# Optimization experiments

Hardware: AMD Instinct MI355X
Metric: run time of the kernel (lower is better)

Reference implementation:

```python
import jax, jax.numpy as jnp
import numpy as np

N = 65536
WAVE_SPEED = 1.0


def _mlp(pt, Ws, bs):
    # pt: [4] -> scalar. 6 tanh hidden layers of width 128, linear head.
    h = pt
    for W, b in zip(Ws[:-1], bs[:-1]):
        h = jnp.tanh(W @ h + b)
    return (Ws[-1] @ h + bs[-1])[0]


def setup_inputs() -> dict:
    key = jax.random.key(0)
    ks = jax.random.split(key, 32)
    d = {}
    for i, name in enumerate(["t", "x", "y", "z"]):
        d[name] = jax.random.normal(ks[i], (N,), dtype=jnp.float32)
    sizes = [(128, 4)] + [(128, 128)] * 5 + [(1, 128)]
    for i, (fan_out, fan_in) in enumerate(sizes):
        # Glorot-like scale for tanh MLP
        scale = np.float32(1.0 / np.sqrt(fan_in))
        d[f"W{i}"] = jax.random.normal(ks[4 + i], (fan_out, fan_in), dtype=jnp.float32) * scale
        d[f"b{i}"] = jnp.zeros((fan_out,), dtype=jnp.float32)
    return d


def reference(t, x, y, z, W0, b0, W1, b1, W2, b2, W3, b3, W4, b4, W5, b5, W6, b6):
    Ws = [W0, W1, W2, W3, W4, W5, W6]
    bs = [b0, b1, b2, b3, b4, b5, b6]

    def u(pt):
        return _mlp(pt, Ws, bs)

    def residual_point(pt):
        # Full 4x4 Hessian via forward-over-reverse; we need only the diagonal.
        H = jax.hessian(u)(pt)  # [4, 4]
        u_tt = H[0, 0]
        laplacian = H[1, 1] + H[2, 2] + H[3, 3]
        return u_tt - (WAVE_SPEED ** 2) * laplacian

    pts = jnp.stack([t, x, y, z], axis=-1)  # [N, 4]
    return jax.vmap(residual_point)(pts)  # [N]
```

## Files before the change

### kernel.cpp

```cpp
#include <hip/hip_runtime.h>
#include <hip/hip_fp16.h>
#include <math.h>


typedef _Float16 f16x8 __attribute__((ext_vector_type(8)));
typedef _Float16 f16x4 __attribute__((ext_vector_type(4)));
typedef _Float16 f16x2 __attribute__((ext_vector_type(2)));
typedef float    f32x4 __attribute__((ext_vector_type(4)));

constexpr int TPB  = 256;
constexpr int P    = 16;
constexpr int H    = 128;
constexpr int XPAD = 136;
constexpr int NV   = 6;
constexpr int WFRAG_HALVES = 5 * 8 * 4 * 64 * 8;
constexpr size_t WS_NEEDED = 2 * WFRAG_HALVES * sizeof(_Float16);

__device__ __forceinline__ float fast_tanh(float v) {
    float e = __expf(-2.0f * fabsf(v));
    float r = __builtin_amdgcn_rcpf(1.0f + e);
    return copysignf((1.0f - e) * r, v);
}

__device__ __forceinline__ f16x2 pkrtz(float a, float b) {
    return __builtin_bit_cast(f16x2, __builtin_amdgcn_cvt_pkrtz(a, b));
}

__global__ __launch_bounds__(256) void presplit_w(
    const float* __restrict__ W1, const float* __restrict__ W2,
    const float* __restrict__ W3, const float* __restrict__ W4,
    const float* __restrict__ W5, _Float16* __restrict__ whi,
    _Float16* __restrict__ wlo)
{
    const int gid = blockIdx.x * 256 + threadIdx.x;
    const float* Ws[5] = { W1, W2, W3, W4, W5 };
    const int lane = gid & 63;
    const int rest = gid >> 6;
    const int ks   = rest & 3;
    const int mt   = (rest >> 2) & 7;
    const int l    = rest >> 5;
    const int n    = mt * 16 + (lane & 15);
    const int k0   = ks * 32 + (lane >> 4) * 8;
    const float4 u0 = *(const float4*)&Ws[l][n * H + k0];
    const float4 u1 = *(const float4*)&Ws[l][n * H + k0 + 4];
    const float vv[8] = { u0.x, u0.y, u0.z, u0.w, u1.x, u1.y, u1.z, u1.w };
    f16x8 h, o;
    #pragma unroll
    for (int e = 0; e < 8; ++e) {
        _Float16 hh = (_Float16)vv[e];
        h[e] = hh;
        o[e] = (_Float16)(vv[e] - (float)hh);
    }
    *(f16x8*)&whi[gid * 8] = h;
    *(f16x8*)&wlo[gid * 8] = o;
}

__global__ __launch_bounds__(TPB, 3) void pinn_mfma5(
    const float* __restrict__ t, const float* __restrict__ x,
    const float* __restrict__ y, const float* __restrict__ z,
    const float* __restrict__ W0, const float* __restrict__ b0,
    const float* __restrict__ W1, const float* __restrict__ b1,
    const float* __restrict__ W2, const float* __restrict__ b2,
    const float* __restrict__ W3, const float* __restrict__ b3,
    const float* __restrict__ W4, const float* __restrict__ b4,
    const float* __restrict__ W5, const float* __restrict__ b5,
    const float* __restrict__ W6,
    const _Float16* __restrict__ whi, const _Float16* __restrict__ wlo,
    int use_pre, float* __restrict__ out, int N)
{
    __shared__ _Float16 sXhi[NV * P * XPAD];
    __shared__ _Float16 sXlo[NV * P * XPAD];
    __shared__ float    sRed[4][P];

    const int tid  = threadIdx.x;
    const int lane = tid & 63;
    const int wn   = tid >> 6;
    const int l15  = lane & 15;
    const int l4   = lane >> 4;
    const int gb   = blockIdx.x * P;

    {
        const int p0 = tid >> 4;
        const int i0 = tid & 15;
        int gp = gb + p0; if (gp >= N) gp = N - 1;
        const float pt0 = t[gp], pt1 = x[gp], pt2 = y[gp], pt3 = z[gp];
        float nv[NV][8];
        #pragma unroll
        for (int j = 0; j < 8; ++j) {
            const int i = i0 * 8 + j;
            const float4 wv = *(const float4*)&W0[i * 4];
            const float zv = fmaf(wv.x, pt0, fmaf(wv.y, pt1, fmaf(wv.z, pt2, fmaf(wv.w, pt3, b0[i]))));
            const float hv = fast_tanh(zv);
            const float s  = 1.0f - hv * hv;
            const float ssq = ((wv.x * wv.x - wv.y * wv.y) - wv.z * wv.z) - wv.w * wv.w;
            nv[0][j] = hv;       nv[1][j] = s * wv.x; nv[2][j] = s * wv.y;
            nv[3][j] = s * wv.z; nv[4][j] = s * wv.w; nv[5][j] = -2.0f * hv * s * ssq;
        }
        #pragma unroll
        for (int v = 0; v < NV; ++v) {
            f16x8 hh, oo;
            #pragma unroll
            for (int j = 0; j < 8; ++j) {
                _Float16 h_ = (_Float16)nv[v][j];
                hh[j] = h_;
                oo[j] = (_Float16)(nv[v][j] - (float)h_);
            }
            const int off = (v * P + p0) * XPAD + i0 * 8;
            *(f16x8*)&sXhi[off] = hh;
            *(f16x8*)&sXlo[off] = oo;
        }
    }
    __syncthreads();

    const float* Wl[5] = { W1, W2, W3, W4, W5 };
    const float* bl[5] = { b1, b2, b3, b4, b5 };

    for (int l = 0; l < 5; ++l) {
        f32x4 acc[NV][2];
        #pragma unroll
        for (int v = 0; v < NV; ++v)
            #pragma unroll
            for (int nt = 0; nt < 2; ++nt) acc[v][nt] = (f32x4){0.f, 0.f, 0.f, 0.f};

        const float* __restrict__ Wc = Wl[l];

        #pragma unroll
        for (int ks = 0; ks < 4; ++ks) {
            f16x8 ah[2], al[2];
            if (use_pre) {
                #pragma unroll
                for (int nt = 0; nt < 2; ++nt) {
                    const int f = ((l * 8 + (wn * 2 + nt)) * 4 + ks) * 64 + lane;
                    ah[nt] = *(const f16x8*)&whi[f * 8];
                    al[nt] = *(const f16x8*)&wlo[f * 8];
                }
            } else {
                #pragma unroll
                for (int nt = 0; nt < 2; ++nt) {
                    const int n  = (wn * 2 + nt) * 16 + l15;
                    const int k0 = ks * 32 + l4 * 8;
                    const float4 u0 = *(const float4*)&Wc[n * H + k0];
                    const float4 u1 = *(const float4*)&Wc[n * H + k0 + 4];
                    const float vv[8] = { u0.x, u0.y, u0.z, u0.w, u1.x, u1.y, u1.z, u1.w };
                    #pragma unroll
                    for (int e = 0; e < 8; ++e) {
                        _Float16 h_ = (_Float16)vv[e];
                        ah[nt][e] = h_;
                        al[nt][e] = (_Float16)(vv[e] - (float)h_);
                    }
                }
            }
            f16x8 xh[NV], xl[NV];
            #pragma unroll
            for (int v = 0; v < NV; ++v) {
                const int base = (v * P + l15) * XPAD + ks * 32 + l4 * 8;
                xh[v] = *(const f16x8*)&sXhi[base];
                xl[v] = *(const f16x8*)&sXlo[base];
            }
            __builtin_amdgcn_s_setprio(1);
            #pragma unroll
            for (int v = 0; v < NV; ++v)
                #pragma unroll
                for (int nt = 0; nt < 2; ++nt)
                    acc[v][nt] = __builtin_amdgcn_mfma_f32_16x16x32_f16(ah[nt], xh[v], acc[v][nt], 0, 0, 0);
            #pragma unroll
            for (int v = 0; v < NV; ++v)
                #pragma unroll
                for (int nt = 0; nt < 2; ++nt)
                    acc[v][nt] = __builtin_amdgcn_mfma_f32_16x16x32_f16(ah[nt], xl[v], acc[v][nt], 0, 0, 0);
            #pragma unroll
            for (int v = 0; v < NV; ++v)
                #pragma unroll
                for (int nt = 0; nt < 2; ++nt)
                    acc[v][nt] = __builtin_amdgcn_mfma_f32_16x16x32_f16(al[nt], xh[v], acc[v][nt], 0, 0, 0);
            __builtin_amdgcn_s_setprio(0);
        }
        __syncthreads();

        if (l < 4) {
            const float* __restrict__ bc = bl[l];
            #pragma unroll
            for (int nt = 0; nt < 2; ++nt) {
                const int n0 = (wn * 2 + nt) * 16 + l4 * 4;
                const float4 b4v = *(const float4*)&bc[n0];
                const float bb[4] = { b4v.x, b4v.y, b4v.z, b4v.w };
                float nv[NV][4];
                #pragma unroll
                for (int r = 0; r < 4; ++r) {
                    const float zv = acc[0][nt][r] + bb[r];
                    const float hv = fast_tanh(zv);
                    const float s  = 1.0f - hv * hv;
                    const float d0 = acc[1][nt][r], d1 = acc[2][nt][r];
                    const float d2 = acc[3][nt][r], d3 = acc[4][nt][r];
                    const float ssq = ((d0 * d0 - d1 * d1) - d2 * d2) - d3 * d3;
                    const float qn  = fmaf(s, acc[5][nt][r], -2.0f * hv * s * ssq);
                    nv[0][r] = hv;     nv[1][r] = s * d0; nv[2][r] = s * d1;
                    nv[3][r] = s * d2; nv[4][r] = s * d3; nv[5][r] = qn;
                }
                #pragma unroll
                for (int v = 0; v < NV; ++v) {
                    const f16x2 h01 = pkrtz(nv[v][0], nv[v][1]);
                    const f16x2 h23 = pkrtz(nv[v][2], nv[v][3]);
                    const float o0 = nv[v][0] - (float)h01[0];
                    const float o1 = nv[v][1] - (float)h01[1];
                    const float o2 = nv[v][2] - (float)h23[0];
                    const float o3 = nv[v][3] - (float)h23[1];
                    const f16x2 o01 = pkrtz(o0, o1);
                    const f16x2 o23 = pkrtz(o2, o3);
                    const int off = (v * P + l15) * XPAD + n0;
                    *(f16x4*)&sXhi[off] = __builtin_shufflevector(h01, h23, 0, 1, 2, 3);
                    *(f16x4*)&sXlo[off] = __builtin_shufflevector(o01, o23, 0, 1, 2, 3);
                }
            }
            __syncthreads();
        } else {
            const float* __restrict__ bc = bl[4];
            float part = 0.0f;
            #pragma unroll
            for (int nt = 0; nt < 2; ++nt) {
                const int n0 = (wn * 2 + nt) * 16 + l4 * 4;
                const float4 b4v = *(const float4*)&bc[n0];
                const float4 w6v = *(const float4*)&W6[n0];
                const float bb[4] = { b4v.x, b4v.y, b4v.z, b4v.w };
                const float ww[4] = { w6v.x, w6v.y, w6v.z, w6v.w };
                #pragma unroll
                for (int r = 0; r < 4; ++r) {
                    const float zv = acc[0][nt][r] + bb[r];
                    const float hv = fast_tanh(zv);
                    const float s  = 1.0f - hv * hv;
                    const float d0 = acc[1][nt][r], d1 = acc[2][nt][r];
                    const float d2 = acc[3][nt][r], d3 = acc[4][nt][r];
                    const float ssq = ((d0 * d0 - d1 * d1) - d2 * d2) - d3 * d3;
                    const float qf  = fmaf(s, acc[5][nt][r], -2.0f * hv * s * ssq);
                    part = fmaf(ww[r], qf, part);
                }
            }
            part += __shfl_xor(part, 16, 64);
            part += __shfl_xor(part, 32, 64);
            if (lane < 16) sRed[wn][lane] = part;
        }
    }

    __syncthreads();
    if (tid < P) {
        const float rsum = sRed[0][tid] + sRed[1][tid] + sRed[2][tid] + sRed[3][tid];
        const int o = gb + tid;
        if (o < N) out[o] = rsum;
    }
}

extern "C" void kernel_launch(void* const* d_in, const int* in_sizes, int n_in,
                              void* d_out, int out_size, void* d_ws, size_t ws_size,
                              hipStream_t stream) {
    const float* t  = (const float*)d_in[0];
    const float* x  = (const float*)d_in[1];
    const float* y  = (const float*)d_in[2];
    const float* z  = (const float*)d_in[3];
    const float* W0 = (const float*)d_in[4];
    const float* b0 = (const float*)d_in[5];
    const float* W1 = (const float*)d_in[6];
    const float* b1 = (const float*)d_in[7];
    const float* W2 = (const float*)d_in[8];
    const float* b2 = (const float*)d_in[9];
    const float* W3 = (const float*)d_in[10];
    const float* b3 = (const float*)d_in[11];
    const float* W4 = (const float*)d_in[12];
    const float* b4 = (const float*)d_in[13];
    const float* W5 = (const float*)d_in[14];
    const float* b5 = (const float*)d_in[15];
    const float* W6 = (const float*)d_in[16];

    const int N = in_sizes[0];
    float* out = (float*)d_out;

    const int use_pre = (ws_size >= WS_NEEDED) ? 1 : 0;
    _Float16* whi = (_Float16*)d_ws;
    _Float16* wlo = whi + WFRAG_HALVES;

    if (use_pre) {
        presplit_w<<<(5 * 8 * 4 * 64) / 256, 256, 0, stream>>>(W1, W2, W3, W4, W5, whi, wlo);
    }
    const int grid = (N + P - 1) / P;
    pinn_mfma5<<<grid, TPB, 0, stream>>>(
        t, x, y, z, W0, b0, W1, b1, W2, b2, W3, b3, W4, b4, W5, b5, W6,
        whi, wlo, use_pre, out, N);
}
```

Baseline: 177.9 us.

## Stagger two point-groups per block so MFMA and tanh phases overlap

Each block now runs 512 threads as two independent groups of 16 points, each with its own LDS buffers. The group's work is split into alternating MFMA and activation stages, and group 1 runs one stage behind group 0. While one group does matrix multiplies the other does tanh and fp16 splitting, which is meant to hide activation latency behind matrix-core work. The cost is doubled LDS per block, a lower occupancy bound (2 blocks of 512), and a block-wide barrier at every stage, including idle stages for each group at the ends.

Measured after the change: 198.4 us. 1.11x slower.

```diff
diff --git a/kernel.cpp b/kernel.cpp
--- a/kernel.cpp
+++ b/kernel.cpp
@@ -8,8 +8,10 @@
 typedef _Float16 f16x2 __attribute__((ext_vector_type(2)));
 typedef float    f32x4 __attribute__((ext_vector_type(4)));
 
-constexpr int TPB  = 256;
-constexpr int P    = 16;
+constexpr int TPB  = 512;
+constexpr int PG   = 16;
+constexpr int NG   = 2;
+constexpr int PB   = PG * NG;
 constexpr int H    = 128;
 constexpr int XPAD = 136;
 constexpr int NV   = 6;
@@ -55,7 +57,7 @@
     *(f16x8*)&wlo[gid * 8] = o;
 }
 
-__global__ __launch_bounds__(TPB, 3) void pinn_mfma5(
+__global__ __launch_bounds__(TPB, 2) void pinn_mfma6(
     const float* __restrict__ t, const float* __restrict__ x,
     const float* __restrict__ y, const float* __restrict__ z,
     const float* __restrict__ W0, const float* __restrict__ b0,
@@ -68,21 +70,27 @@
     const _Float16* __restrict__ whi, const _Float16* __restrict__ wlo,
     int use_pre, float* __restrict__ out, int N)
 {
-    __shared__ _Float16 sXhi[NV * P * XPAD];
-    __shared__ _Float16 sXlo[NV * P * XPAD];
-    __shared__ float    sRed[4][P];
+    __shared__ _Float16 sXhi[NG][NV * PG * XPAD];
+    __shared__ _Float16 sXlo[NG][NV * PG * XPAD];
+    __shared__ float    sRed[NG][4][PG];
 
     const int tid  = threadIdx.x;
     const int lane = tid & 63;
-    const int wn   = tid >> 6;
+    const int wave = tid >> 6;
+    const int g    = wave >> 2;
+    const int wn   = wave & 3;
     const int l15  = lane & 15;
     const int l4   = lane >> 4;
-    const int gb   = blockIdx.x * P;
+    const int gb   = blockIdx.x * PB;
+
+    _Float16* __restrict__ myXhi = &sXhi[g][0];
+    _Float16* __restrict__ myXlo = &sXlo[g][0];
 
     {
-        const int p0 = tid >> 4;
-        const int i0 = tid & 15;
-        int gp = gb + p0; if (gp >= N) gp = N - 1;
+        const int gt = tid & 255;
+        const int p0 = gt >> 4;
+        const int i0 = gt & 15;
+        int gp = gb + g * PG + p0; if (gp >= N) gp = N - 1;
         const float pt0 = t[gp], pt1 = x[gp], pt2 = y[gp], pt3 = z[gp];
         float nv[NV][8];
         #pragma unroll
@@ -105,145 +113,147 @@
                 hh[j] = h_;
                 oo[j] = (_Float16)(nv[v][j] - (float)h_);
             }
-            const int off = (v * P + p0) * XPAD + i0 * 8;
-            *(f16x8*)&sXhi[off] = hh;
-            *(f16x8*)&sXlo[off] = oo;
+            const int off = (v * PG + p0) * XPAD + i0 * 8;
+            *(f16x8*)&myXhi[off] = hh;
+            *(f16x8*)&myXlo[off] = oo;
         }
     }
     __syncthreads();
 
-    const float* Wl[5] = { W1, W2, W3, W4, W5 };
-    const float* bl[5] = { b1, b2, b3, b4, b5 };
-
-    for (int l = 0; l < 5; ++l) {
-        f32x4 acc[NV][2];
-        #pragma unroll
-        for (int v = 0; v < NV; ++v)
-            #pragma unroll
-            for (int nt = 0; nt < 2; ++nt) acc[v][nt] = (f32x4){0.f, 0.f, 0.f, 0.f};
-
-        const float* __restrict__ Wc = Wl[l];
-
-        #pragma unroll
-        for (int ks = 0; ks < 4; ++ks) {
-            f16x8 ah[2], al[2];
-            if (use_pre) {
+    f32x4 acc[NV][2];
+
+    for (int s = 0; s < 11; ++s) {
+        const int u = s - g;
+        if (u >= 0 && u < 10) {
+            const int l = u >> 1;
+            if ((u & 1) == 0) {
+                #pragma unroll
+                for (int v = 0; v < NV; ++v)
+                    #pragma unroll
+                    for (int nt = 0; nt < 2; ++nt) acc[v][nt] = (f32x4){0.f, 0.f, 0.f, 0.f};
+
+                const float* __restrict__ Wc =
+                    (l == 0) ? W1 : (l == 1) ? W2 : (l == 2) ? W3 : (l == 3) ? W4 : W5;
+
+                #pragma unroll
+                for (int ks = 0; ks < 4; ++ks) {
+                    f16x8 ah[2], al[2];
+                    if (use_pre) {
+                        #pragma unroll
+                        for (int nt = 0; nt < 2; ++nt) {
+                            const int f = ((l * 8 + (wn * 2 + nt)) * 4 + ks) * 64 + lane;
+                            ah[nt] = *(const f16x8*)&whi[f * 8];
+                            al[nt] = *(const f16x8*)&wlo[f * 8];
+                        }
+                    } else {
+                        #pragma unroll
+                        for (int nt = 0; nt < 2; ++nt) {
+                            const int n  = (wn * 2 + nt) * 16 + l15;
+                            const int k0 = ks * 32 + l4 * 8;
+                            const float4 u0 = *(const float4*)&Wc[n * H + k0];
+                            const float4 u1 = *(const float4*)&Wc[n * H + k0 + 4];
+                            const float vv[8] = { u0.x, u0.y, u0.z, u0.w, u1.x, u1.y, u1.z, u1.w };
+                            #pragma unroll
+                            for (int e = 0; e < 8; ++e) {
+                                _Float16 h_ = (_Float16)vv[e];
+                                ah[nt][e] = h_;
+                                al[nt][e] = (_Float16)(vv[e] - (float)h_);
+                            }
+                        }
+                    }
+                    f16x8 xh[NV], xl[NV];
+                    #pragma unroll
+                    for (int v = 0; v < NV; ++v) {
+                        const int base = (v * PG + l15) * XPAD + ks * 32 + l4 * 8;
+                        xh[v] = *(const f16x8*)&myXhi[base];
+                        xl[v] = *(const f16x8*)&myXlo[base];
+                    }
+                    __builtin_amdgcn_s_setprio(1);
+                    #pragma unroll
+                    for (int v = 0; v < NV; ++v)
+                        #pragma unroll
+                        for (int nt = 0; nt < 2; ++nt)
+                            acc[v][nt] = __builtin_amdgcn_mfma_f32_16x16x32_f16(ah[nt], xh[v], acc[v][nt], 0, 0, 0);
+                    #pragma unroll
+                    for (int v = 0; v < NV; ++v)
+                        #pragma unroll
+                        for (int nt = 0; nt < 2; ++nt)
+                            acc[v][nt] = __builtin_amdgcn_mfma_f32_16x16x32_f16(ah[nt], xl[v], acc[v][nt], 0, 0, 0);
+                    #pragma unroll
+                    for (int v = 0; v < NV; ++v)
+                        #pragma unroll
+                        for (int nt = 0; nt < 2; ++nt)
+                            acc[v][nt] = __builtin_amdgcn_mfma_f32_16x16x32_f16(al[nt], xh[v], acc[v][nt], 0, 0, 0);
+                    __builtin_amdgcn_s_setprio(0);
+                }
+            } else if (l < 4) {
+                const float* __restrict__ bc =
+                    (l == 0) ? b1 : (l == 1) ? b2 : (l == 2) ? b3 : b4;
                 #pragma unroll
                 for (int nt = 0; nt < 2; ++nt) {
-                    const int f = ((l * 8 + (wn * 2 + nt)) * 4 + ks) * 64 + lane;
-                    ah[nt] = *(const f16x8*)&whi[f * 8];
-                    al[nt] = *(const f16x8*)&wlo[f * 8];
+                    const int n0 = (wn * 2 + nt) * 16 + l4 * 4;
+                    const float4 b4v = *(const float4*)&bc[n0];
+                    const float bb[4] = { b4v.x, b4v.y, b4v.z, b4v.w };
+                    float nv[NV][4];
+                    #pragma unroll
+                    for (int r = 0; r < 4; ++r) {
+                        const float zv = acc[0][nt][r] + bb[r];
+                        const float hv = fast_tanh(zv);
+                        const float s  = 1.0f - hv * hv;
+                        const float d0 = acc[1][nt][r], d1 = acc[2][nt][r];
+                        const float d2 = acc[3][nt][r], d3 = acc[4][nt][r];
+                        const float ssq = ((d0 * d0 - d1 * d1) - d2 * d2) - d3 * d3;
+                        const float qn  = fmaf(s, acc[5][nt][r], -2.0f * hv * s * ssq);
+                        nv[0][r] = hv;     nv[1][r] = s * d0; nv[2][r] = s * d1;
+                        nv[3][r] = s * d2; nv[4][r] = s * d3; nv[5][r] = qn;
+                    }
+                    #pragma unroll
+                    for (int v = 0; v < NV; ++v) {
+                        const f16x2 h01 = pkrtz(nv[v][0], nv[v][1]);
+                        const f16x2 h23 = pkrtz(nv[v][2], nv[v][3]);
+                        const float o0 = nv[v][0] - (float)h01[0];
+                        const float o1 = nv[v][1] - (float)h01[1];
+                        const float o2 = nv[v][2] - (float)h23[0];
+                        const float o3 = nv[v][3] - (float)h23[1];
+                        const f16x2 o01 = pkrtz(o0, o1);
+                        const f16x2 o23 = pkrtz(o2, o3);
+                        const int off = (v * PG + l15) * XPAD + n0;
+                        *(f16x4*)&myXhi[off] = __builtin_shufflevector(h01, h23, 0, 1, 2, 3);
+                        *(f16x4*)&myXlo[off] = __builtin_shufflevector(o01, o23, 0, 1, 2, 3);
+                    }
                 }
             } else {
+                float part = 0.0f;
                 #pragma unroll
                 for (int nt = 0; nt < 2; ++nt) {
-                    const int n  = (wn * 2 + nt) * 16 + l15;
-                    const int k0 = ks * 32 + l4 * 8;
-                    const float4 u0 = *(const float4*)&Wc[n * H + k0];
-                    const float4 u1 = *(const float4*)&Wc[n * H + k0 + 4];
-                    const float vv[8] = { u0.x, u0.y, u0.z, u0.w, u1.x, u1.y, u1.z, u1.w };
-                    #pragma unroll
-                    for (int e = 0; e < 8; ++e) {
-                        _Float16 h_ = (_Float16)vv[e];
-                        ah[nt][e] = h_;
-                        al[nt][e] = (_Float16)(vv[e] - (float)h_);
+                    const int n0 = (wn * 2 + nt) * 16 + l4 * 4;
+                    const float4 b4v = *(const float4*)&b5[n0];
+                    const float4 w6v = *(const float4*)&W6[n0];
+                    const float bb[4] = { b4v.x, b4v.y, b4v.z, b4v.w };
+                    const float ww[4] = { w6v.x, w6v.y, w6v.z, w6v.w };
+                    #pragma unroll
+                    for (int r = 0; r < 4; ++r) {
+                        const float zv = acc[0][nt][r] + bb[r];
+                        const float hv = fast_tanh(zv);
+                        const float s  = 1.0f - hv * hv;
+                        const float d0 = acc[1][nt][r], d1 = acc[2][nt][r];
+                        const float d2 = acc[3][nt][r], d3 = acc[4][nt][r];
+                        const float ssq = ((d0 * d0 - d1 * d1) - d2 * d2) - d3 * d3;
+                        const float qf  = fmaf(s, acc[5][nt][r], -2.0f * hv * s * ssq);
+                        part = fmaf(ww[r], qf, part);
                     }
                 }
+                part += __shfl_xor(part, 16, 64);
+                part += __shfl_xor(part, 32, 64);
+                if (lane < 16) sRed[g][wn][lane] = part;
             }
-            f16x8 xh[NV], xl[NV];
-            #pragma unroll
-            for (int v = 0; v < NV; ++v) {
-                const int base = (v * P + l15) * XPAD + ks * 32 + l4 * 8;
-                xh[v] = *(const f16x8*)&sXhi[base];
-                xl[v] = *(const f16x8*)&sXlo[base];
-            }
-            __builtin_amdgcn_s_setprio(1);
-            #pragma unroll
-            for (int v = 0; v < NV; ++v)
-                #pragma unroll
-                for (int nt = 0; nt < 2; ++nt)
-                    acc[v][nt] = __builtin_amdgcn_mfma_f32_16x16x32_f16(ah[nt], xh[v], acc[v][nt], 0, 0, 0);
-            #pragma unroll
-            for (int v = 0; v < NV; ++v)
-                #pragma unroll
-                for (int nt = 0; nt < 2; ++nt)
-                    acc[v][nt] = __builtin_amdgcn_mfma_f32_16x16x32_f16(ah[nt], xl[v], acc[v][nt], 0, 0, 0);
-            #pragma unroll
-            for (int v = 0; v < NV; ++v)
-                #pragma unroll
-                for (int nt = 0; nt < 2; ++nt)
-                    acc[v][nt] = __builtin_amdgcn_mfma_f32_16x16x32_f16(al[nt], xh[v], acc[v][nt], 0, 0, 0);
-            __builtin_amdgcn_s_setprio(0);
         }
         __syncthreads();
-
-        if (l < 4) {
-            const float* __restrict__ bc = bl[l];
-            #pragma unroll
-            for (int nt = 0; nt < 2; ++nt) {
-                const int n0 = (wn * 2 + nt) * 16 + l4 * 4;
-                const float4 b4v = *(const float4*)&bc[n0];
-                const float bb[4] = { b4v.x, b4v.y, b4v.z, b4v.w };
-                float nv[NV][4];
-                #pragma unroll
-                for (int r = 0; r < 4; ++r) {
-                    const float zv = acc[0][nt][r] + bb[r];
-                    const float hv = fast_tanh(zv);
-                    const float s  = 1.0f - hv * hv;
-                    const float d0 = acc[1][nt][r], d1 = acc[2][nt][r];
-                    const float d2 = acc[3][nt][r], d3 = acc[4][nt][r];
-                    const float ssq = ((d0 * d0 - d1 * d1) - d2 * d2) - d3 * d3;
-                    const float qn  = fmaf(s, acc[5][nt][r], -2.0f * hv * s * ssq);
-                    nv[0][r] = hv;     nv[1][r] = s * d0; nv[2][r] = s * d1;
-                    nv[3][r] = s * d2; nv[4][r] = s * d3; nv[5][r] = qn;
-                }
-                #pragma unroll
-                for (int v = 0; v < NV; ++v) {
-                    const f16x2 h01 = pkrtz(nv[v][0], nv[v][1]);
-                    const f16x2 h23 = pkrtz(nv[v][2], nv[v][3]);
-                    const float o0 = nv[v][0] - (float)h01[0];
-                    const float o1 = nv[v][1] - (float)h01[1];
-                    const float o2 = nv[v][2] - (float)h23[0];
-                    const float o3 = nv[v][3] - (float)h23[1];
-                    const f16x2 o01 = pkrtz(o0, o1);
-                    const f16x2 o23 = pkrtz(o2, o3);
-                    const int off = (v * P + l15) * XPAD + n0;
-                    *(f16x4*)&sXhi[off] = __builtin_shufflevector(h01, h23, 0, 1, 2, 3);
-                    *(f16x4*)&sXlo[off] = __builtin_shufflevector(o01, o23, 0, 1, 2, 3);
-                }
-            }
-            __syncthreads();
-        } else {
-            const float* __restrict__ bc = bl[4];
-            float part = 0.0f;
-            #pragma unroll
-            for (int nt = 0; nt < 2; ++nt) {
-                const int n0 = (wn * 2 + nt) * 16 + l4 * 4;
-                const float4 b4v = *(const float4*)&bc[n0];
-                const float4 w6v = *(const float4*)&W6[n0];
-                const float bb[4] = { b4v.x, b4v.y, b4v.z, b4v.w };
-                const float ww[4] = { w6v.x, w6v.y, w6v.z, w6v.w };
-                #pragma unroll
-                for (int r = 0; r < 4; ++r) {
-                    const float zv = acc[0][nt][r] + bb[r];
-                    const float hv = fast_tanh(zv);
-                    const float s  = 1.0f - hv * hv;
-                    const float d0 = acc[1][nt][r], d1 = acc[2][nt][r];
-                    const float d2 = acc[3][nt][r], d3 = acc[4][nt][r];
-                    const float ssq = ((d0 * d0 - d1 * d1) - d2 * d2) - d3 * d3;
-                    const float qf  = fmaf(s, acc[5][nt][r], -2.0f * hv * s * ssq);
-                    part = fmaf(ww[r], qf, part);
-                }
-            }
-            part += __shfl_xor(part, 16, 64);
-            part += __shfl_xor(part, 32, 64);
-            if (lane < 16) sRed[wn][lane] = part;
-        }
-    }
-
-    __syncthreads();
-    if (tid < P) {
-        const float rsum = sRed[0][tid] + sRed[1][tid] + sRed[2][tid] + sRed[3][tid];
+    }
+
+    if (tid < PB) {
+        const int g2 = tid >> 4, p = tid & 15;
+        const float rsum = sRed[g2][0][p] + sRed[g2][1][p] + sRed[g2][2][p] + sRed[g2][3][p];
         const int o = gb + tid;
         if (o < N) out[o] = rsum;
     }
@@ -280,8 +290,8 @@
     if (use_pre) {
         presplit_w<<<(5 * 8 * 4 * 64) / 256, 256, 0, stream>>>(W1, W2, W3, W4, W5, whi, wlo);
     }
-    const int grid = (N + P - 1) / P;
-    pinn_mfma5<<<grid, TPB, 0, stream>>>(
+    const int grid = (N + PB - 1) / PB;
+    pinn_mfma6<<<grid, TPB, 0, stream>>>(
         t, x, y, z, W0, b0, W1, b1, W2, b2, W3, b3, W4, b4, W5, b5, W6,
         whi, wlo, use_pre, out, N);
 }
```
